# Kernel tuning notes

Measured on AMD Instinct MI355X. Metric: run time of the kernel, lower is better.

## Reference

```python
import jax, jax.numpy as jnp
import numpy as np

NUM_CODES = 1296
D_DIM = 64


def setup_inputs() -> dict:
    key = jax.random.key(0)
    k1, k2 = jax.random.split(key)
    inputs = jax.random.normal(k1, (32, 64, 64, D_DIM), dtype=jnp.float32)
    # lecun_normal init: stddev = 1/sqrt(fan_in) with fan_in = d
    embeddings = jax.random.normal(k2, (NUM_CODES, D_DIM), dtype=jnp.float32) / np.sqrt(D_DIM)
    return {"inputs": inputs, "embeddings": embeddings}


def reference(inputs, embeddings):
    x1 = jnp.sum(inputs ** 2, axis=-1, keepdims=True)          # [b,m,n,1]
    x2 = jnp.sum(embeddings ** 2, axis=-1)                      # [k]
    x3 = jnp.einsum('bmnd,kd->bmnk', inputs, embeddings)        # [b,m,n,k]
    D = x1 + x2 - 2.0 * x3
    codes = jnp.argmin(D, axis=-1).astype(jnp.int32)            # [b,m,n]
    code_vecs = embeddings[codes]                               # [b,m,n,d]
    return codes, code_vecs
```

## Files before the change

### kernel.cpp

```cpp
#include <hip/hip_runtime.h>

#define NUM_CODES 1296
#define PAD_CODES 1344
#define DDIM 64
#define NUM_Q 131072
#define THREADS 256
#define WAVES 4
#define QPW 32
#define QPB 128
#define MARGIN 0.25f
#define SLOTS 16
#define CHUNK 96
#define NSTEP 14

typedef __attribute__((ext_vector_type(8))) short bf16x8;
typedef __attribute__((ext_vector_type(4))) float f32x4;

__device__ __forceinline__ ushort f2bf(float f) {
    unsigned u = __float_as_uint(f);
    return (ushort)((u + 0x7fffu + ((u >> 16) & 1u)) >> 16);
}

__device__ __forceinline__ void gl_lds(const ushort* g, ushort* l) {
    __builtin_amdgcn_global_load_lds(
        (const __attribute__((address_space(1))) unsigned int*)(g),
        (__attribute__((address_space(3))) unsigned int*)(l), 16, 0, 0);
}

#define DPPMIN(v, ctrl) { \
    int t_ = __builtin_amdgcn_update_dpp(0, __float_as_int(v), ctrl, 0xf, 0xf, true); \
    v = fminf(v, __int_as_float(t_)); }
#define DPPRED16(v) { DPPMIN(v, 0xB1) DPPMIN(v, 0x4E) DPPMIN(v, 0x141) DPPMIN(v, 0x140) }

__global__ __launch_bounds__(64) void vq_prep(const float* __restrict__ emb,
                                              float* __restrict__ enorm,
                                              ushort* __restrict__ eh) {
    int k = blockIdx.x * 64 + threadIdx.x;
    if (k >= PAD_CODES) return;
    int ks = k < NUM_CODES ? k : NUM_CODES - 1;
    const float* e = emb + (size_t)ks * DDIM;
    float f[DDIM];
#pragma unroll
    for (int i = 0; i < 16; ++i) {
        float4 v = *(const float4*)(e + 4 * i);
        f[4*i] = v.x; f[4*i+1] = v.y; f[4*i+2] = v.z; f[4*i+3] = v.w;
    }
    {
#pragma clang fp contract(off)
        float r8[8];
#pragma unroll
        for (int j = 0; j < 8; ++j) { float t = f[j] * f[j]; r8[j] = t; }
#pragma unroll
        for (int i = 1; i < 8; ++i) {
#pragma unroll
            for (int j = 0; j < 8; ++j) { float t = f[i*8+j] * f[i*8+j]; r8[j] += t; }
        }
        enorm[k] = ((r8[0]+r8[1])+(r8[2]+r8[3])) + ((r8[4]+r8[5])+(r8[6]+r8[7]));
    }
    ushort h[DDIM];
#pragma unroll
    for (int d = 0; d < DDIM; ++d) h[d] = f2bf(f[d]);
    uint* dh = (uint*)(eh + (size_t)k * DDIM);
#pragma unroll
    for (int s = 0; s < 8; ++s) {
        int ds = s ^ (k & 7);
#pragma unroll
        for (int j = 0; j < 4; ++j)
            dh[ds*4 + j] = (uint)h[s*8 + 2*j] | ((uint)h[s*8 + 2*j + 1] << 16);
    }
}

__global__ __launch_bounds__(256) void vq_xnorm(const float* __restrict__ x,
                                                float* __restrict__ xnorm) {
    int q = blockIdx.x * 256 + threadIdx.x;
    const float* r = x + (size_t)q * DDIM;
    float f[DDIM];
#pragma unroll
    for (int i = 0; i < 16; ++i) {
        float4 v = *(const float4*)(r + 4 * i);
        f[4*i] = v.x; f[4*i+1] = v.y; f[4*i+2] = v.z; f[4*i+3] = v.w;
    }
    {
#pragma clang fp contract(off)
        float r8[8];
#pragma unroll
        for (int j = 0; j < 8; ++j) { float t = f[j] * f[j]; r8[j] = t; }
#pragma unroll
        for (int i = 1; i < 8; ++i) {
#pragma unroll
            for (int j = 0; j < 8; ++j) { float t = f[i*8+j] * f[i*8+j]; r8[j] += t; }
        }
        xnorm[q] = ((r8[0]+r8[1])+(r8[2]+r8[3])) + ((r8[4]+r8[5])+(r8[6]+r8[7]));
    }
}

__global__ __launch_bounds__(THREADS) void vq_main(
        const float* __restrict__ x, const float* __restrict__ emb,
        const float* __restrict__ enorm_g, const float* __restrict__ xnorm,
        const ushort* __restrict__ eh, float* __restrict__ out) {
    __shared__ ushort sbuf[2][CHUNK * DDIM];
    __shared__ ushort wq[WAVES][QPW * SLOTS];
    __shared__ unsigned qcnt[WAVES][QPW];
    __shared__ unsigned skk[WAVES][QPW];

    const int tid  = threadIdx.x;
    const int lane = tid & 63;
    const int w    = tid >> 6;
    const int cl   = lane & 15;
    const int g    = lane >> 4;
    const long qw  = (long)blockIdx.x * QPB + w * QPW;

    if (lane < QPW) qcnt[w][lane] = 0;

    bf16x8 a00, a01, a10, a11;
    {
        const float* xp0 = x + (qw + cl) * DDIM + g * 8;
        const float* xp1 = xp0 + 16 * DDIM;
#pragma unroll
        for (int j = 0; j < 8; ++j) {
            a00[j] = (short)f2bf(xp0[j]);
            a01[j] = (short)f2bf(xp0[j + 32]);
            a10[j] = (short)f2bf(xp1[j]);
            a11[j] = (short)f2bf(xp1[j + 32]);
        }
    }

    float rmin0[4], rmin1[4];
#pragma unroll
    for (int r = 0; r < 4; ++r) { rmin0[r] = __builtin_inff(); rmin1[r] = __builtin_inff(); }

    const int slot0 = (g     ^ (cl & 7)) * 8;
    const int slot1 = ((g+4) ^ (cl & 7)) * 8;
    const f32x4 z4 = {0.f, 0.f, 0.f, 0.f};

    {
#pragma unroll
        for (int k = 0; k < 3; ++k)
            gl_lds(eh + (size_t)(k * THREADS + tid) * 8,
                   &sbuf[0][(size_t)(k * THREADS + tid) * 8]);
    }
    __syncthreads();

#define MFMA_TILE(T, D0, D1) { \
        const ushort* bp_ = &sbuf[cur][(size_t)((T) * 16 + cl) * DDIM]; \
        bf16x8 b0_ = *(const bf16x8*)(bp_ + slot0); \
        bf16x8 b1_ = *(const bf16x8*)(bp_ + slot1); \
        D0 = __builtin_amdgcn_mfma_f32_16x16x32_bf16(a00, b0_, z4, 0, 0, 0); \
        D1 = __builtin_amdgcn_mfma_f32_16x16x32_bf16(a10, b0_, z4, 0, 0, 0); \
        D0 = __builtin_amdgcn_mfma_f32_16x16x32_bf16(a01, b1_, D0, 0, 0, 0); \
        D1 = __builtin_amdgcn_mfma_f32_16x16x32_bf16(a11, b1_, D1, 0, 0, 0); }

#define SCORE_TILE(T, D0, D1) { \
        float en_ = en[T]; \
        _Pragma("unroll") \
        for (int r = 0; r < 4; ++r) { \
            D0[r] = fmaf(-2.f, D0[r], en_); \
            D1[r] = fmaf(-2.f, D1[r], en_); \
            rmin0[r] = fminf(rmin0[r], D0[r]); \
            rmin1[r] = fminf(rmin1[r], D1[r]); } }

#define TEST_TILE(T, D0, D1) { \
        const int c_ = cb + (T) * 16 + cl; \
        if (c_ < NUM_CODES) { \
            _Pragma("unroll") \
            for (int r = 0; r < 4; ++r) { \
                if (D0[r] <= thr0[r]) { \
                    unsigned i_ = atomicAdd(&qcnt[w][g*4 + r], 1u); \
                    if (i_ < SLOTS) wq[w][(g*4 + r) * SLOTS + i_] = (ushort)c_; } \
                if (D1[r] <= thr1[r]) { \
                    unsigned i_ = atomicAdd(&qcnt[w][16 + g*4 + r], 1u); \
                    if (i_ < SLOTS) wq[w][(16 + g*4 + r) * SLOTS + i_] = (ushort)c_; } } } }

    int cur = 0;
    for (int s = 0; s < NSTEP; ++s) {
        const bool more = (s + 1 < NSTEP);
        if (more) {
            const ushort* src = eh + (size_t)(s + 1) * CHUNK * DDIM;
#pragma unroll
            for (int k = 0; k < 3; ++k)
                gl_lds(src + (size_t)(k * THREADS + tid) * 8,
                       &sbuf[cur ^ 1][(size_t)(k * THREADS + tid) * 8]);
        }
        const int cb = s * CHUNK;
        float en[6];
#pragma unroll
        for (int t = 0; t < 6; ++t) en[t] = enorm_g[cb + t * 16 + cl];

        f32x4 d00, d01, d02, d03, d04, d05;
        f32x4 d10, d11, d12, d13, d14, d15;
        MFMA_TILE(0, d00, d10); MFMA_TILE(1, d01, d11); MFMA_TILE(2, d02, d12);
        MFMA_TILE(3, d03, d13); MFMA_TILE(4, d04, d14); MFMA_TILE(5, d05, d15);
        SCORE_TILE(0, d00, d10); SCORE_TILE(1, d01, d11); SCORE_TILE(2, d02, d12);
        SCORE_TILE(3, d03, d13); SCORE_TILE(4, d04, d14); SCORE_TILE(5, d05, d15);
#pragma unroll
        for (int r = 0; r < 4; ++r) { DPPRED16(rmin0[r]); DPPRED16(rmin1[r]); }
        float thr0[4], thr1[4];
#pragma unroll
        for (int r = 0; r < 4; ++r) { thr0[r] = rmin0[r] + MARGIN; thr1[r] = rmin1[r] + MARGIN; }
        TEST_TILE(0, d00, d10); TEST_TILE(1, d01, d11); TEST_TILE(2, d02, d12);
        TEST_TILE(3, d03, d13); TEST_TILE(4, d04, d14); TEST_TILE(5, d05, d15);
        __syncthreads();
        cur ^= 1;
    }

    auto exact_pk = [&](int c, long gq) -> unsigned long long {
        const float* xr = x + gq * DDIM;
        const float* er = emb + (size_t)c * DDIM;
        float dot = 0.f;
#pragma unroll
        for (int p4 = 0; p4 < 16; ++p4) {
            float4 xv = *(const float4*)(xr + 4 * p4);
            float4 ev = *(const float4*)(er + 4 * p4);
            dot = fmaf(xv.x, ev.x, dot); dot = fmaf(xv.y, ev.y, dot);
            dot = fmaf(xv.z, ev.z, dot); dot = fmaf(xv.w, ev.w, dot);
        }
        float dist = (xnorm[gq] + enorm_g[c]) - 2.f * dot;
        unsigned u = __float_as_uint(dist);
        unsigned key = (u & 0x80000000u) ? ~u : (u | 0x80000000u);
        return ((unsigned long long)key << 32) | (unsigned)c;
    };

    const int grp = lane >> 3, gl = lane & 7;
#pragma unroll
    for (int qo = 0; qo < 4; ++qo) {
        const int ql = qo * 8 + grp;
        const long gq = qw + ql;
        const unsigned nq = qcnt[w][ql];
        unsigned long long pk = ~0ULL;
        if (nq <= SLOTS) {
            for (unsigned i = gl; i < nq; i += 8) {
                unsigned long long t = exact_pk((int)wq[w][ql * SLOTS + i], gq);
                if (t < pk) pk = t;
            }
        }
#pragma unroll
        for (int m = 1; m < 8; m <<= 1) {
            unsigned long long o = (unsigned long long)__shfl_xor((long long)pk, m, 64);
            if (o < pk) pk = o;
        }
        if (gl == 0 && nq <= SLOTS) {
            skk[w][ql] = (unsigned)pk;
            out[gq] = (float)(unsigned)pk;
        }
    }
    for (int ql = 0; ql < QPW; ++ql) {
        if (qcnt[w][ql] <= SLOTS) continue;
        const long gq = qw + ql;
        unsigned long long pk = ~0ULL;
        for (int t = 0; t < 21; ++t) {
            int c = lane + (t << 6);
            if (c < NUM_CODES) {
                unsigned long long tp = exact_pk(c, gq);
                if (tp < pk) pk = tp;
            }
        }
#pragma unroll
        for (int m = 1; m < 64; m <<= 1) {
            unsigned long long o = (unsigned long long)__shfl_xor((long long)pk, m, 64);
            if (o < pk) pk = o;
        }
        if (lane == 0) {
            skk[w][ql] = (unsigned)pk;
            out[gq] = (float)(unsigned)pk;
        }
    }

    const int gu = lane >> 4, gv = lane & 15;
#pragma unroll
    for (int qo = 0; qo < 8; ++qo) {
        const int ql = qo * 4 + gu;
        const unsigned kk = skk[w][ql];
        const long gq = qw + ql;
        *(float4*)(out + (long)NUM_Q + gq * DDIM + gv * 4) =
            *(const float4*)(emb + (size_t)kk * DDIM + gv * 4);
    }
}

extern "C" void kernel_launch(void* const* d_in, const int* in_sizes, int n_in,
                              void* d_out, int out_size, void* d_ws, size_t ws_size,
                              hipStream_t stream) {
    const float* x   = (const float*)d_in[0];
    const float* emb = (const float*)d_in[1];
    float*  enorm = (float*)d_ws;
    float*  xnorm = (float*)((char*)d_ws + 8192);
    ushort* eh    = (ushort*)((char*)d_ws + 532480);

    hipLaunchKernelGGL(vq_prep, dim3(PAD_CODES / 64), dim3(64), 0, stream,
                       emb, enorm, eh);
    hipLaunchKernelGGL(vq_xnorm, dim3(NUM_Q / 256), dim3(256), 0, stream,
                       x, xnorm);
    hipLaunchKernelGGL(vq_main, dim3(NUM_Q / QPB), dim3(THREADS), 0, stream,
                       x, emb, enorm, xnorm, eh, (float*)d_out);
}
```

Baseline: 144.2 us.

## Keep whole bf16 codebook resident in LDS and drop per-chunk barriers

The 512-thread block now loads the first 1280 bf16 codes into LDS once, replacing the double-buffered 96-code chunks that needed a barrier each step. The last 16 codes are held in registers and handled as a separate tile. Candidate lists and counts move from LDS to global workspace so the 160KB LDS buffer fits. The embedding gather is fused into the refine step. The cost is much lower occupancy (one block per CU) and global atomics for candidate collection instead of LDS atomics.

```diff
diff --git a/kernel.cpp b/kernel.cpp
--- a/kernel.cpp
+++ b/kernel.cpp
@@ -1,17 +1,16 @@
 #include <hip/hip_runtime.h>
 
 #define NUM_CODES 1296
-#define PAD_CODES 1344
+#define LDSC 1280
 #define DDIM 64
 #define NUM_Q 131072
-#define THREADS 256
-#define WAVES 4
+#define THREADS 512
+#define WAVES 8
 #define QPW 32
-#define QPB 128
+#define QPB 256
 #define MARGIN 0.25f
 #define SLOTS 16
-#define CHUNK 96
-#define NSTEP 14
+#define NGRP 10
 
 typedef __attribute__((ext_vector_type(8))) short bf16x8;
 typedef __attribute__((ext_vector_type(4))) float f32x4;
@@ -36,9 +35,8 @@
                                               float* __restrict__ enorm,
                                               ushort* __restrict__ eh) {
     int k = blockIdx.x * 64 + threadIdx.x;
-    if (k >= PAD_CODES) return;
-    int ks = k < NUM_CODES ? k : NUM_CODES - 1;
-    const float* e = emb + (size_t)ks * DDIM;
+    if (k >= NUM_CODES) return;
+    const float* e = emb + (size_t)k * DDIM;
     float f[DDIM];
 #pragma unroll
     for (int i = 0; i < 16; ++i) {
@@ -97,20 +95,23 @@
 __global__ __launch_bounds__(THREADS) void vq_main(
         const float* __restrict__ x, const float* __restrict__ emb,
         const float* __restrict__ enorm_g, const float* __restrict__ xnorm,
-        const ushort* __restrict__ eh, float* __restrict__ out) {
-    __shared__ ushort sbuf[2][CHUNK * DDIM];
-    __shared__ ushort wq[WAVES][QPW * SLOTS];
-    __shared__ unsigned qcnt[WAVES][QPW];
-    __shared__ unsigned skk[WAVES][QPW];
-
+        const ushort* __restrict__ eh, ushort* __restrict__ wq_g,
+        unsigned* __restrict__ qcnt_g, float* __restrict__ out) {
+    __shared__ ushort sbuf[LDSC * DDIM];
     const int tid  = threadIdx.x;
     const int lane = tid & 63;
     const int w    = tid >> 6;
     const int cl   = lane & 15;
     const int g    = lane >> 4;
     const long qw  = (long)blockIdx.x * QPB + w * QPW;
-
-    if (lane < QPW) qcnt[w][lane] = 0;
+    const long qb0 = (long)blockIdx.x * QPB;
+
+    for (int i = tid; i < QPB; i += THREADS) qcnt_g[qb0 + i] = 0;
+
+#pragma unroll
+    for (int u = 0; u < 20; ++u)
+        gl_lds(eh + (size_t)(u * THREADS + tid) * 8,
+               &sbuf[(size_t)(u * THREADS + tid) * 8]);
 
     bf16x8 a00, a01, a10, a11;
     {
@@ -125,24 +126,27 @@
         }
     }
 
-    float rmin0[4], rmin1[4];
-#pragma unroll
-    for (int r = 0; r < 4; ++r) { rmin0[r] = __builtin_inff(); rmin1[r] = __builtin_inff(); }
-
     const int slot0 = (g     ^ (cl & 7)) * 8;
     const int slot1 = ((g+4) ^ (cl & 7)) * 8;
     const f32x4 z4 = {0.f, 0.f, 0.f, 0.f};
 
-    {
-#pragma unroll
-        for (int k = 0; k < 3; ++k)
-            gl_lds(eh + (size_t)(k * THREADS + tid) * 8,
-                   &sbuf[0][(size_t)(k * THREADS + tid) * 8]);
-    }
+    bf16x8 t80b0, t80b1;
+    float en80;
+    {
+        const ushort* ep = eh + (size_t)(LDSC + cl) * DDIM;
+        t80b0 = *(const bf16x8*)(ep + slot0);
+        t80b1 = *(const bf16x8*)(ep + slot1);
+        en80 = enorm_g[LDSC + cl];
+    }
+
+    float rmin0[4], rmin1[4];
+#pragma unroll
+    for (int r = 0; r < 4; ++r) { rmin0[r] = __builtin_inff(); rmin1[r] = __builtin_inff(); }
+
     __syncthreads();
 
-#define MFMA_TILE(T, D0, D1) { \
-        const ushort* bp_ = &sbuf[cur][(size_t)((T) * 16 + cl) * DDIM]; \
+#define MFMA_T(TT, D0, D1) { \
+        const ushort* bp_ = &sbuf[(size_t)((TT) * 16 + cl) * DDIM]; \
         bf16x8 b0_ = *(const bf16x8*)(bp_ + slot0); \
         bf16x8 b1_ = *(const bf16x8*)(bp_ + slot1); \
         D0 = __builtin_amdgcn_mfma_f32_16x16x32_bf16(a00, b0_, z4, 0, 0, 0); \
@@ -150,7 +154,7 @@
         D0 = __builtin_amdgcn_mfma_f32_16x16x32_bf16(a01, b1_, D0, 0, 0, 0); \
         D1 = __builtin_amdgcn_mfma_f32_16x16x32_bf16(a11, b1_, D1, 0, 0, 0); }
 
-#define SCORE_TILE(T, D0, D1) { \
+#define SCORE_T(T, D0, D1) { \
         float en_ = en[T]; \
         _Pragma("unroll") \
         for (int r = 0; r < 4; ++r) { \
@@ -159,48 +163,61 @@
             rmin0[r] = fminf(rmin0[r], D0[r]); \
             rmin1[r] = fminf(rmin1[r], D1[r]); } }
 
-#define TEST_TILE(T, D0, D1) { \
-        const int c_ = cb + (T) * 16 + cl; \
-        if (c_ < NUM_CODES) { \
-            _Pragma("unroll") \
-            for (int r = 0; r < 4; ++r) { \
-                if (D0[r] <= thr0[r]) { \
-                    unsigned i_ = atomicAdd(&qcnt[w][g*4 + r], 1u); \
-                    if (i_ < SLOTS) wq[w][(g*4 + r) * SLOTS + i_] = (ushort)c_; } \
-                if (D1[r] <= thr1[r]) { \
-                    unsigned i_ = atomicAdd(&qcnt[w][16 + g*4 + r], 1u); \
-                    if (i_ < SLOTS) wq[w][(16 + g*4 + r) * SLOTS + i_] = (ushort)c_; } } } }
-
-    int cur = 0;
-    for (int s = 0; s < NSTEP; ++s) {
-        const bool more = (s + 1 < NSTEP);
-        if (more) {
-            const ushort* src = eh + (size_t)(s + 1) * CHUNK * DDIM;
-#pragma unroll
-            for (int k = 0; k < 3; ++k)
-                gl_lds(src + (size_t)(k * THREADS + tid) * 8,
-                       &sbuf[cur ^ 1][(size_t)(k * THREADS + tid) * 8]);
-        }
-        const int cb = s * CHUNK;
-        float en[6];
-#pragma unroll
-        for (int t = 0; t < 6; ++t) en[t] = enorm_g[cb + t * 16 + cl];
-
-        f32x4 d00, d01, d02, d03, d04, d05;
-        f32x4 d10, d11, d12, d13, d14, d15;
-        MFMA_TILE(0, d00, d10); MFMA_TILE(1, d01, d11); MFMA_TILE(2, d02, d12);
-        MFMA_TILE(3, d03, d13); MFMA_TILE(4, d04, d14); MFMA_TILE(5, d05, d15);
-        SCORE_TILE(0, d00, d10); SCORE_TILE(1, d01, d11); SCORE_TILE(2, d02, d12);
-        SCORE_TILE(3, d03, d13); SCORE_TILE(4, d04, d14); SCORE_TILE(5, d05, d15);
+#define TEST_T(CC, D0, D1) { \
+        const int c_ = (CC); \
+        _Pragma("unroll") \
+        for (int r = 0; r < 4; ++r) { \
+            if (D0[r] <= thr0[r]) { \
+                unsigned i_ = atomicAdd(&qcnt_g[qw + g*4 + r], 1u); \
+                if (i_ < SLOTS) wq_g[(size_t)(qw + g*4 + r) * SLOTS + i_] = (ushort)c_; } \
+            if (D1[r] <= thr1[r]) { \
+                unsigned i_ = atomicAdd(&qcnt_g[qw + 16 + g*4 + r], 1u); \
+                if (i_ < SLOTS) wq_g[(size_t)(qw + 16 + g*4 + r) * SLOTS + i_] = (ushort)c_; } } }
+
+    for (int gi = 0; gi < NGRP; ++gi) {
+        const int tb = gi * 8;
+        const int cb = tb * 16;
+        float en[8];
+#pragma unroll
+        for (int t = 0; t < 8; ++t) en[t] = enorm_g[cb + t * 16 + cl];
+        f32x4 d00, d01, d02, d03, d04, d05, d06, d07;
+        f32x4 d10, d11, d12, d13, d14, d15, d16, d17;
+        MFMA_T(tb + 0, d00, d10); MFMA_T(tb + 1, d01, d11);
+        MFMA_T(tb + 2, d02, d12); MFMA_T(tb + 3, d03, d13);
+        MFMA_T(tb + 4, d04, d14); MFMA_T(tb + 5, d05, d15);
+        MFMA_T(tb + 6, d06, d16); MFMA_T(tb + 7, d07, d17);
+        SCORE_T(0, d00, d10); SCORE_T(1, d01, d11); SCORE_T(2, d02, d12);
+        SCORE_T(3, d03, d13); SCORE_T(4, d04, d14); SCORE_T(5, d05, d15);
+        SCORE_T(6, d06, d16); SCORE_T(7, d07, d17);
 #pragma unroll
         for (int r = 0; r < 4; ++r) { DPPRED16(rmin0[r]); DPPRED16(rmin1[r]); }
         float thr0[4], thr1[4];
 #pragma unroll
         for (int r = 0; r < 4; ++r) { thr0[r] = rmin0[r] + MARGIN; thr1[r] = rmin1[r] + MARGIN; }
-        TEST_TILE(0, d00, d10); TEST_TILE(1, d01, d11); TEST_TILE(2, d02, d12);
-        TEST_TILE(3, d03, d13); TEST_TILE(4, d04, d14); TEST_TILE(5, d05, d15);
-        __syncthreads();
-        cur ^= 1;
+        TEST_T(cb + 0*16 + cl, d00, d10); TEST_T(cb + 1*16 + cl, d01, d11);
+        TEST_T(cb + 2*16 + cl, d02, d12); TEST_T(cb + 3*16 + cl, d03, d13);
+        TEST_T(cb + 4*16 + cl, d04, d14); TEST_T(cb + 5*16 + cl, d05, d15);
+        TEST_T(cb + 6*16 + cl, d06, d16); TEST_T(cb + 7*16 + cl, d07, d17);
+    }
+    {
+        f32x4 d0, d1;
+        d0 = __builtin_amdgcn_mfma_f32_16x16x32_bf16(a00, t80b0, z4, 0, 0, 0);
+        d1 = __builtin_amdgcn_mfma_f32_16x16x32_bf16(a10, t80b0, z4, 0, 0, 0);
+        d0 = __builtin_amdgcn_mfma_f32_16x16x32_bf16(a01, t80b1, d0, 0, 0, 0);
+        d1 = __builtin_amdgcn_mfma_f32_16x16x32_bf16(a11, t80b1, d1, 0, 0, 0);
+#pragma unroll
+        for (int r = 0; r < 4; ++r) {
+            d0[r] = fmaf(-2.f, d0[r], en80);
+            d1[r] = fmaf(-2.f, d1[r], en80);
+            rmin0[r] = fminf(rmin0[r], d0[r]);
+            rmin1[r] = fminf(rmin1[r], d1[r]);
+        }
+#pragma unroll
+        for (int r = 0; r < 4; ++r) { DPPRED16(rmin0[r]); DPPRED16(rmin1[r]); }
+        float thr0[4], thr1[4];
+#pragma unroll
+        for (int r = 0; r < 4; ++r) { thr0[r] = rmin0[r] + MARGIN; thr1[r] = rmin1[r] + MARGIN; }
+        TEST_T(LDSC + cl, d0, d1);
     }
 
     auto exact_pk = [&](int c, long gq) -> unsigned long long {
@@ -225,26 +242,28 @@
     for (int qo = 0; qo < 4; ++qo) {
         const int ql = qo * 8 + grp;
         const long gq = qw + ql;
-        const unsigned nq = qcnt[w][ql];
+        const unsigned nq = qcnt_g[gq];
         unsigned long long pk = ~0ULL;
         if (nq <= SLOTS) {
             for (unsigned i = gl; i < nq; i += 8) {
-                unsigned long long t = exact_pk((int)wq[w][ql * SLOTS + i], gq);
+                unsigned long long t = exact_pk((int)wq_g[gq * SLOTS + i], gq);
                 if (t < pk) pk = t;
             }
-        }
-#pragma unroll
-        for (int m = 1; m < 8; m <<= 1) {
-            unsigned long long o = (unsigned long long)__shfl_xor((long long)pk, m, 64);
-            if (o < pk) pk = o;
-        }
-        if (gl == 0 && nq <= SLOTS) {
-            skk[w][ql] = (unsigned)pk;
-            out[gq] = (float)(unsigned)pk;
+#pragma unroll
+            for (int m = 1; m < 8; m <<= 1) {
+                unsigned long long o = (unsigned long long)__shfl_xor((long long)pk, m, 64);
+                if (o < pk) pk = o;
+            }
+            const unsigned kk = (unsigned)pk;
+            if (gl == 0) out[gq] = (float)kk;
+#pragma unroll
+            for (int j = 0; j < 2; ++j)
+                *(float4*)(out + (long)NUM_Q + gq * DDIM + (gl * 2 + j) * 4) =
+                    *(const float4*)(emb + (size_t)kk * DDIM + (gl * 2 + j) * 4);
         }
     }
     for (int ql = 0; ql < QPW; ++ql) {
-        if (qcnt[w][ql] <= SLOTS) continue;
+        if (qcnt_g[qw + ql] <= SLOTS) continue;
         const long gq = qw + ql;
         unsigned long long pk = ~0ULL;
         for (int t = 0; t < 21; ++t) {
@@ -259,20 +278,11 @@
             unsigned long long o = (unsigned long long)__shfl_xor((long long)pk, m, 64);
             if (o < pk) pk = o;
         }
-        if (lane == 0) {
-            skk[w][ql] = (unsigned)pk;
-            out[gq] = (float)(unsigned)pk;
-        }
-    }
-
-    const int gu = lane >> 4, gv = lane & 15;
-#pragma unroll
-    for (int qo = 0; qo < 8; ++qo) {
-        const int ql = qo * 4 + gu;
-        const unsigned kk = skk[w][ql];
-        const long gq = qw + ql;
-        *(float4*)(out + (long)NUM_Q + gq * DDIM + gv * 4) =
-            *(const float4*)(emb + (size_t)kk * DDIM + gv * 4);
+        const unsigned kk = (unsigned)pk;
+        if (lane == 0) out[gq] = (float)kk;
+        if (lane < 16)
+            *(float4*)(out + (long)NUM_Q + gq * DDIM + lane * 4) =
+                *(const float4*)(emb + (size_t)kk * DDIM + lane * 4);
     }
 }
 
@@ -281,14 +291,16 @@
                               hipStream_t stream) {
     const float* x   = (const float*)d_in[0];
     const float* emb = (const float*)d_in[1];
-    float*  enorm = (float*)d_ws;
-    float*  xnorm = (float*)((char*)d_ws + 8192);
-    ushort* eh    = (ushort*)((char*)d_ws + 532480);
-
-    hipLaunchKernelGGL(vq_prep, dim3(PAD_CODES / 64), dim3(64), 0, stream,
+    float*    enorm = (float*)d_ws;
+    float*    xnorm = (float*)((char*)d_ws + 8192);
+    ushort*   eh    = (ushort*)((char*)d_ws + 532480);
+    ushort*   wq_g  = (ushort*)((char*)d_ws + 702464);
+    unsigned* qcnt  = (unsigned*)((char*)d_ws + 4896768);
+
+    hipLaunchKernelGGL(vq_prep, dim3((NUM_CODES + 63) / 64), dim3(64), 0, stream,
                        emb, enorm, eh);
     hipLaunchKernelGGL(vq_xnorm, dim3(NUM_Q / 256), dim3(256), 0, stream,
                        x, xnorm);
     hipLaunchKernelGGL(vq_main, dim3(NUM_Q / QPB), dim3(THREADS), 0, stream,
-                       x, emb, enorm, xnorm, eh, (float*)d_out);
-}
+                       x, emb, enorm, xnorm, eh, wq_g, qcnt, (float*)d_out);
+}
```

New measurement: 212.8 us. 1.48x slower.
